# Kernel tuning notes

Hardware: AMD Instinct MI355X
Metric: run time of the kernel (lower is better)

Reference implementation:

```python
import jax, jax.numpy as jnp
import numpy as np

B, N, PS = 8, 2048, 32
P = N // PS          # 64 patches
D, MLP, DEPTH, H, DH = 1024, 2048, 6, 8, 64
INNER = H * DH       # 512
K = 20
EPS = 1e-5


def setup_inputs() -> dict:
    key = jax.random.key(0)
    ks = jax.random.split(key, 16)
    r = lambda i, shape: jax.random.normal(ks[i], shape, dtype=jnp.float32) * 0.02
    return {
        "x": jax.random.normal(ks[0], (B, N, 3), dtype=jnp.float32),
        "x_pos_embed": r(1, (B, P + 1, D)),
        "w1": r(2, (64, 6)),   "g1": jnp.ones(64),  "b1": jnp.zeros(64),
        "w2": r(3, (64, 128)), "g2": jnp.ones(64),  "b2": jnp.zeros(64),
        "w3": r(4, (128, 128)),"g3": jnp.ones(128), "b3": jnp.zeros(128),
        "w4": r(5, (256, 256)),"g4": jnp.ones(256), "b4": jnp.zeros(256),
        "w5": r(6, (D, 512)),  "g5": jnp.ones(D),   "b5": jnp.zeros(D),
        "cls_token": r(7, (1, 1, D)),
        "ln1_g": jnp.ones((DEPTH, D)), "ln1_b": jnp.zeros((DEPTH, D)),
        "wqkv": r(8, (DEPTH, D, 3 * INNER)),
        "wout": r(9, (DEPTH, INNER, D)), "bout": jnp.zeros((DEPTH, D)),
        "ln2_g": jnp.ones((DEPTH, D)), "ln2_b": jnp.zeros((DEPTH, D)),
        "wff1": r(10, (DEPTH, D, MLP)), "bff1": jnp.zeros((DEPTH, MLP)),
        "wff2": r(11, (DEPTH, MLP, D)), "bff2": jnp.zeros((DEPTH, D)),
    }


def _knn(x, k):  # x: [B, C, N] -> neighbor idx [B, N, k]
    xx = jnp.sum(x * x, axis=1)                        # [B, N]
    inner = jnp.einsum('bcn,bcm->bnm', x, x)           # [B, N, N]
    dist = 2.0 * inner - xx[:, :, None] - xx[:, None, :]  # = -||xi-xj||^2
    return jax.lax.top_k(dist, k)[1]


def _graph_feature(x, k):  # x: [B, C, N] -> [B, N, k, 2C]
    idx = _knn(x, k)
    xt = jnp.transpose(x, (0, 2, 1))                   # [B, N, C]
    nbr = jax.vmap(lambda f, i: f[i])(xt, idx)         # gather: [B, N, k, C]
    ctr = jnp.broadcast_to(xt[:, :, None, :], nbr.shape)
    return jnp.concatenate([nbr - ctr, ctr], axis=-1)


def _leaky(v):
    return jnp.where(v >= 0, v, 0.2 * v)


def _edge_conv(x, w, g, b, k):  # EdgeConv block: graph feat -> 1x1 conv -> BN(train) -> lrelu -> max over k
    f = _graph_feature(x, k)                           # [B, N, k, 2C]
    y = jnp.einsum('bnkc,oc->bonk', f, w)              # [B, O, N, k]
    mu = jnp.mean(y, axis=(0, 2, 3), keepdims=True)
    var = jnp.var(y, axis=(0, 2, 3), keepdims=True)
    y = (y - mu) * jax.lax.rsqrt(var + EPS) * g[None, :, None, None] + b[None, :, None, None]
    return jnp.max(_leaky(y), axis=-1)                 # [B, O, N]


def _ln(x, g, b):
    mu = jnp.mean(x, axis=-1, keepdims=True)
    var = jnp.var(x, axis=-1, keepdims=True)
    return (x - mu) * jax.lax.rsqrt(var + EPS) * g + b


def reference(x, x_pos_embed, w1, g1, b1, w2, g2, b2, w3, g3, b3, w4, g4, b4,
              w5, g5, b5, cls_token, ln1_g, ln1_b, wqkv, wout, bout,
              ln2_g, ln2_b, wff1, bff1, wff2, bff2):
    scale = DH ** -0.5
    pts = jnp.transpose(x, (0, 2, 1))                  # [B, 3, N]
    x1 = _edge_conv(pts, w1, g1, b1, K)                # [B, 64, N]
    x2 = _edge_conv(x1, w2, g2, b2, K)                 # [B, 64, N]
    x3 = _edge_conv(x2, w3, g3, b3, K)                 # [B, 128, N]
    x4 = _edge_conv(x3, w4, g4, b4, K)                 # [B, 256, N]
    h = jnp.concatenate([x1, x2, x3, x4], axis=1)      # [B, 512, N]
    y = jnp.einsum('bcn,oc->bon', h, w5)               # conv5 1x1 -> [B, D, N]
    mu = jnp.mean(y, axis=(0, 2), keepdims=True)
    var = jnp.var(y, axis=(0, 2), keepdims=True)
    y = _leaky((y - mu) * jax.lax.rsqrt(var + EPS) * g5[None, :, None] + b5[None, :, None])
    # patch max-pool: 'b (p n) c -> (b p) n c' then max over n
    t = jnp.transpose(y, (0, 2, 1)).reshape(B * P, PS, D)
    t = jnp.max(t, axis=1).reshape(B, P, D)
    t = jnp.concatenate([jnp.broadcast_to(cls_token, (B, 1, D)), t], axis=1)  # [B, P+1, D]
    for i in range(DEPTH):
        t = t + x_pos_embed
        hn = _ln(t, ln1_g[i], ln1_b[i])
        qkv = (hn @ wqkv[i]).reshape(B, P + 1, 3, H, DH)
        q, k_, v = [jnp.transpose(qkv[:, :, j], (0, 2, 1, 3)) for j in range(3)]
        attn = jax.nn.softmax(jnp.einsum('bhld,bhmd->bhlm', q, k_) * scale, axis=-1)
        z = jnp.einsum('bhlm,bhmd->bhld', attn, v)
        z = jnp.transpose(z, (0, 2, 1, 3)).reshape(B, P + 1, INNER)
        t = t + z @ wout[i] + bout[i]
        hn = _ln(t, ln2_g[i], ln2_b[i])
        t = t + jax.nn.gelu(hn @ wff1[i] + bff1[i], approximate=False) @ wff2[i] + bff2[i]
    return t[:, 1:]                                    # [B, P, D]
```

## Files before the change

kernel.cpp:

```cpp
#include <hip/hip_runtime.h>
#include <math.h>

#define BB 8
#define NN 2048
#define PSZ 32
#define PP 64
#define DD 1024
#define MLPD 2048
#define DEPTH_ 6
#define HH 8
#define DHH 64
#define INNER_ 512
#define KK 20
#define TOK 65
#define EPSF 1e-5f

#define GEMM_ACC 1
#define GEMM_GELU 2
#define GEMM_OUTBF16 4

typedef __bf16 bf16_t;
typedef __attribute__((ext_vector_type(8))) __bf16 bf16x8;
typedef __attribute__((ext_vector_type(4))) float f32x4;

__global__ void transpose_x_kernel(const float* __restrict__ x, float* __restrict__ pts) {
    int gid = blockIdx.x * blockDim.x + threadIdx.x;
    if (gid >= BB * NN * 3) return;
    int c = gid % 3; int n = (gid / 3) % NN; int b = gid / (3 * NN);
    pts[(b * 3 + c) * NN + n] = x[gid];
}

__global__ void sqnorm_kernel(const float* __restrict__ x, int bs, int C, float* __restrict__ xx) {
    int gid = blockIdx.x * blockDim.x + threadIdx.x;
    if (gid >= BB * NN) return;
    int n = gid % NN; int b = gid / NN;
    const float* xp = x + b * bs + n;
    float s = 0.f;
    for (int c = 0; c < C; ++c) { float v = xp[c * NN]; s += v * v; }
    xx[gid] = s;
}

__global__ __launch_bounds__(256) void dist_kernel(const float* __restrict__ x, int bs, int C,
                                                   const float* __restrict__ xx, int b0,
                                                   float* __restrict__ dist) {
    __shared__ float As[16][72];
    __shared__ float Bs[16][72];
    int b = b0 + blockIdx.z;
    int n0 = blockIdx.y * 64, m0 = blockIdx.x * 64;
    int tid = threadIdx.x;
    int ty = tid / 16, tx = tid % 16;
    float acc[4][4] = {};
    const float* xb = x + (long)b * bs;
    for (int k0 = 0; k0 < C; k0 += 16) {
        for (int ppp = 0; ppp < 4; ++ppp) {
            int li = tid + ppp * 256;
            int i = li % 64, kk = li / 64;
            int c = k0 + kk;
            As[kk][i] = (c < C) ? xb[c * NN + n0 + i] : 0.f;
            Bs[kk][i] = (c < C) ? xb[c * NN + m0 + i] : 0.f;
        }
        __syncthreads();
        for (int kk = 0; kk < 16; ++kk) {
            float a[4], bv[4];
            *(float4*)a = *(const float4*)&As[kk][ty * 4];
            *(float4*)bv = *(const float4*)&Bs[kk][tx * 4];
            for (int i2 = 0; i2 < 4; ++i2)
                for (int j = 0; j < 4; ++j)
                    acc[i2][j] += a[i2] * bv[j];
        }
        __syncthreads();
    }
    float* db = dist + (long)blockIdx.z * NN * NN;
    for (int i2 = 0; i2 < 4; ++i2) {
        int n = n0 + ty * 4 + i2;
        float xn = xx[b * NN + n];
        float4 st;
        int m = m0 + tx * 4;
        st.x = 2.f * acc[i2][0] - xn - xx[b * NN + m + 0];
        st.y = 2.f * acc[i2][1] - xn - xx[b * NN + m + 1];
        st.z = 2.f * acc[i2][2] - xn - xx[b * NN + m + 2];
        st.w = 2.f * acc[i2][3] - xn - xx[b * NN + m + 3];
        *(float4*)&db[(long)n * NN + m] = st;
    }
}

__global__ __launch_bounds__(256) void topk_kernel(const float* __restrict__ dist, int b0,
                                                   int* __restrict__ idx) {
    int b = b0 + blockIdx.y;
    int wid = threadIdx.x >> 6, lane = threadIdx.x & 63;
    int n = blockIdx.x * 4 + wid;
    const float* row = dist + ((long)blockIdx.y * NN + n) * NN;
    float vals[32];
    #pragma unroll
    for (int s = 0; s < 32; ++s) vals[s] = row[s * 64 + lane];
    int* op = idx + ((long)b * NN + n) * KK;
    for (int kk = 0; kk < KK; ++kk) {
        float bv = vals[0]; int bsl = 0;
        #pragma unroll
        for (int s = 1; s < 32; ++s) if (vals[s] > bv) { bv = vals[s]; bsl = s; }
        int bm = bsl * 64 + lane;
        for (int off = 32; off; off >>= 1) {
            float ov = __shfl_xor(bv, off);
            int om = __shfl_xor(bm, off);
            if (ov > bv || (ov == bv && om < bm)) { bv = ov; bm = om; }
        }
        int wslot = bm >> 6, wlane = bm & 63;
        #pragma unroll
        for (int s = 0; s < 32; ++s)
            if (s == wslot) vals[s] = (lane == wlane) ? -INFINITY : vals[s];
        if (lane == 0) op[kk] = bm;
    }
}

__global__ __launch_bounds__(256) void pq_kernel(const float* __restrict__ x, int bs, int C,
                                                 const float* __restrict__ w, int O,
                                                 float* __restrict__ p, float* __restrict__ q) {
    __shared__ float wT[256][33];
    __shared__ float xs[128][32];
    int b = blockIdx.z;
    int o0 = blockIdx.y * 32;
    int n0 = blockIdx.x * 32;
    int tid = threadIdx.x;
    for (int i = tid; i < 2 * C * 32; i += 256) {
        int c2 = i % (2 * C), o = i / (2 * C);
        wT[c2][o] = w[(o0 + o) * 2 * C + c2];
    }
    for (int i = tid; i < C * 32; i += 256) {
        int nl = i % 32, c = i / 32;
        xs[c][nl] = x[b * bs + c * NN + n0 + nl];
    }
    __syncthreads();
    int o_l = tid & 31;
    int n_base = (tid >> 5) * 4;
    float ps[4] = {0.f, 0.f, 0.f, 0.f};
    float qs[4] = {0.f, 0.f, 0.f, 0.f};
    for (int c = 0; c < C; ++c) {
        float4 xv = *(const float4*)&xs[c][n_base];
        float wa = wT[c][o_l];
        float wb = wT[C + c][o_l];
        float d = wb - wa;
        ps[0] += xv.x * wa; qs[0] += xv.x * d;
        ps[1] += xv.y * wa; qs[1] += xv.y * d;
        ps[2] += xv.z * wa; qs[2] += xv.z * d;
        ps[3] += xv.w * wa; qs[3] += xv.w * d;
    }
    for (int j = 0; j < 4; ++j) {
        long r = (long)(b * NN + n0 + n_base + j) * O + o0 + o_l;
        p[r] = ps[j];
        q[r] = qs[j];
    }
}

__global__ void zero_stats_kernel(double* __restrict__ s1, double* __restrict__ s2) {
    int t = blockIdx.x * blockDim.x + threadIdx.x;
    if (t < 1024) { s1[t] = 0.0; s2[t] = 0.0; }
}

__global__ __launch_bounds__(256) void edge_stats_kernel(const float* __restrict__ p, const float* __restrict__ q,
                                                         const int* __restrict__ idx, int O,
                                                         double* __restrict__ gsum, double* __restrict__ gsumsq) {
    int tid = threadIdx.x;
    int o = tid % O;
    int grp = tid / O;
    int ngrp = 256 / O;
    int rows_per_blk = (BB * NN) / gridDim.x;
    int r0 = blockIdx.x * rows_per_blk;
    double s = 0.0, ss = 0.0;
    for (int r = r0 + grp; r < r0 + rows_per_blk; r += ngrp) {
        int b = r / NN;
        float qv = q[r * O + o];
        for (int k = 0; k < KK; ++k) {
            int j = idx[r * KK + k];
            float v = p[(b * NN + j) * O + o] + qv;
            s += v; ss += (double)v * v;
        }
    }
    atomicAdd(&gsum[o], s);
    atomicAdd(&gsumsq[o], ss);
}

__global__ void bn_finalize_kernel(const double* __restrict__ gsum, const double* __restrict__ gsumsq,
                                   const float* __restrict__ g, const float* __restrict__ bb, int O, double cnt,
                                   float* __restrict__ scale, float* __restrict__ shift) {
    int o = blockIdx.x * blockDim.x + threadIdx.x;
    if (o >= O) return;
    double mean = gsum[o] / cnt;
    double var = gsumsq[o] / cnt - mean * mean;
    float inv = rsqrtf((float)var + EPSF);
    float sc = g[o] * inv;
    scale[o] = sc;
    shift[o] = bb[o] - (float)mean * sc;
}

__global__ void edge_out_kernel(const float* __restrict__ p, const float* __restrict__ q,
                                const int* __restrict__ idx, int O,
                                const float* __restrict__ scale, const float* __restrict__ shift,
                                float* __restrict__ out, int obs) {
    int gid = blockIdx.x * blockDim.x + threadIdx.x;
    if (gid >= BB * NN * O) return;
    int o = gid % O; int n = (gid / O) % NN; int b = gid / (O * NN);
    int r = b * NN + n;
    float qv = q[r * O + o];
    float sc = scale[o], sh = shift[o];
    float m = -INFINITY;
    for (int k = 0; k < KK; ++k) {
        int j = idx[r * KK + k];
        float v = (p[(b * NN + j) * O + o] + qv) * sc + sh;
        v = (v >= 0.f) ? v : 0.2f * v;
        m = fmaxf(m, v);
    }
    out[b * obs + o * NN + n] = m;
}

__global__ __launch_bounds__(256) void transpose_cvt_kernel(const float* __restrict__ in,
                                                            bf16_t* __restrict__ outp,
                                                            int R, int C, long s_in, long s_out) {
    __shared__ float tile[32][33];
    const float* ib = in + (long)blockIdx.z * s_in;
    bf16_t* ob = outp + (long)blockIdx.z * s_out;
    int r0 = blockIdx.y * 32, c0 = blockIdx.x * 32;
    int tx = threadIdx.x & 31, tg = threadIdx.x >> 5;
    for (int i = 0; i < 4; ++i) {
        int r = tg + i * 8;
        tile[r][tx] = ib[(long)(r0 + r) * C + c0 + tx];
    }
    __syncthreads();
    for (int i = 0; i < 4; ++i) {
        int c = tg + i * 8;
        ob[(long)(c0 + c) * R + r0 + tx] = (bf16_t)tile[tx][c];
    }
}

__global__ __launch_bounds__(256) void gemm_bf16_kernel(const float* __restrict__ A,
                                                        const bf16_t* __restrict__ Bt,
                                                        const float* __restrict__ bias,
                                                        float* __restrict__ out,
                                                        int M, int Kd, int Nd,
                                                        long sA, long sBt, long sO, int flags) {
    __shared__ __align__(16) bf16_t As[64 * 32];
    __shared__ __align__(16) bf16_t Bs[64 * 32];
    const float* Ab = A + (long)blockIdx.z * sA;
    const bf16_t* Bb = Bt + (long)blockIdx.z * sBt;
    int row0 = blockIdx.y * 64, col0 = blockIdx.x * 64;
    int tid = threadIdx.x;
    int lane = tid & 63, wv = tid >> 6;
    int wm = wv >> 1, wn = wv & 1;
    int srow = tid >> 2;
    int skp = (tid & 3) * 8;
    f32x4 acc[2][2] = {};
    for (int k0 = 0; k0 < Kd; k0 += 32) {
        {
            int r = row0 + srow;
            float av[8];
            if (r < M) {
                const float* ap = Ab + (long)r * Kd + k0 + skp;
                float4 a0 = *(const float4*)ap;
                float4 a1 = *(const float4*)(ap + 4);
                av[0] = a0.x; av[1] = a0.y; av[2] = a0.z; av[3] = a0.w;
                av[4] = a1.x; av[5] = a1.y; av[6] = a1.z; av[7] = a1.w;
            } else {
                #pragma unroll
                for (int j = 0; j < 8; ++j) av[j] = 0.f;
            }
            bf16x8 v;
            #pragma unroll
            for (int j = 0; j < 8; ++j) v[j] = (bf16_t)av[j];
            *(bf16x8*)&As[((skp >> 3) * 64 + srow) * 8] = v;
        }
        {
            const bf16_t* bp = Bb + (long)(col0 + srow) * Kd + k0 + skp;
            bf16x8 v = *(const bf16x8*)bp;
            *(bf16x8*)&Bs[((skp >> 3) * 64 + srow) * 8] = v;
        }
        __syncthreads();
        int q = lane >> 4, cl = lane & 15;
        bf16x8 a0v = *(const bf16x8*)&As[(q * 64 + wm * 32 + cl) * 8];
        bf16x8 a1v = *(const bf16x8*)&As[(q * 64 + wm * 32 + 16 + cl) * 8];
        bf16x8 b0v = *(const bf16x8*)&Bs[(q * 64 + wn * 32 + cl) * 8];
        bf16x8 b1v = *(const bf16x8*)&Bs[(q * 64 + wn * 32 + 16 + cl) * 8];
        acc[0][0] = __builtin_amdgcn_mfma_f32_16x16x32_bf16(a0v, b0v, acc[0][0], 0, 0, 0);
        acc[0][1] = __builtin_amdgcn_mfma_f32_16x16x32_bf16(a0v, b1v, acc[0][1], 0, 0, 0);
        acc[1][0] = __builtin_amdgcn_mfma_f32_16x16x32_bf16(a1v, b0v, acc[1][0], 0, 0, 0);
        acc[1][1] = __builtin_amdgcn_mfma_f32_16x16x32_bf16(a1v, b1v, acc[1][1], 0, 0, 0);
        __syncthreads();
    }
    int q = lane >> 4, cl = lane & 15;
    float* Obf = out + (long)blockIdx.z * sO;
    bf16_t* Obh = (bf16_t*)out + (long)blockIdx.z * sO;
    for (int mt = 0; mt < 2; ++mt)
        for (int nt = 0; nt < 2; ++nt)
            #pragma unroll
            for (int r = 0; r < 4; ++r) {
                int row = row0 + wm * 32 + mt * 16 + q * 4 + r;
                if (row >= M) continue;
                int col = col0 + wn * 32 + nt * 16 + cl;
                float v = acc[mt][nt][r];
                if (bias) v += bias[col];
                if (flags & GEMM_GELU) v = 0.5f * v * (1.f + erff(v * 0.70710678118654752f));
                long oidx = (long)row * Nd + col;
                if (flags & GEMM_OUTBF16) Obh[oidx] = (bf16_t)v;
                else if (flags & GEMM_ACC) Obf[oidx] += v;
                else Obf[oidx] = v;
            }
}

__global__ __launch_bounds__(256) void gemm_kernel(const float* __restrict__ A, const float* __restrict__ Bm,
                                                   const float* __restrict__ bias, float* __restrict__ out,
                                                   int M, int Kd, int Nd, long sA, long sB, long sO, int flags) {
    __shared__ float As[16][65];
    __shared__ float Bs[16][64];
    const float* Ab = A + (long)blockIdx.z * sA;
    const float* Bb = Bm + (long)blockIdx.z * sB;
    float* Ob = out + (long)blockIdx.z * sO;
    int row0 = blockIdx.y * 64, col0 = blockIdx.x * 64;
    int tid = threadIdx.x;
    int ty = tid / 16, tx = tid % 16;
    float acc[4][4] = {};
    for (int k0 = 0; k0 < Kd; k0 += 16) {
        for (int i = 0; i < 4; ++i) {
            int li = tid + i * 256;
            int m = li / 16, kk = li % 16;
            int r = row0 + m;
            As[kk][m] = (r < M) ? Ab[(long)r * Kd + k0 + kk] : 0.f;
        }
        for (int i = 0; i < 4; ++i) {
            int li = tid + i * 256;
            int kk = li / 64, n = li % 64;
            int c = col0 + n;
            Bs[kk][n] = (c < Nd) ? Bb[(long)(k0 + kk) * Nd + c] : 0.f;
        }
        __syncthreads();
        for (int kk = 0; kk < 16; ++kk) {
            float a[4], bv[4];
            for (int i = 0; i < 4; ++i) a[i] = As[kk][ty * 4 + i];
            for (int j = 0; j < 4; ++j) bv[j] = Bs[kk][tx * 4 + j];
            for (int i = 0; i < 4; ++i)
                for (int j = 0; j < 4; ++j)
                    acc[i][j] += a[i] * bv[j];
        }
        __syncthreads();
    }
    for (int i = 0; i < 4; ++i) {
        int r = row0 + ty * 4 + i;
        if (r >= M) continue;
        for (int j = 0; j < 4; ++j) {
            int c = col0 + tx * 4 + j;
            if (c >= Nd) continue;
            float v = acc[i][j];
            if (bias) v += bias[c];
            if (flags & GEMM_GELU) v = 0.5f * v * (1.f + erff(v * 0.70710678118654752f));
            long oidx = (long)r * Nd + c;
            if (flags & GEMM_ACC) Ob[oidx] += v; else Ob[oidx] = v;
        }
    }
}

__global__ __launch_bounds__(256) void bn5_stats_bf16_kernel(const bf16_t* __restrict__ y5,
                                                             const float* __restrict__ g,
                                                             const float* __restrict__ bb,
                                                             float* __restrict__ scale, float* __restrict__ shift) {
    __shared__ double ssum[256], ssq[256];
    int d = blockIdx.x;
    int tid = threadIdx.x;
    double s = 0.0, sq = 0.0;
    for (int b = 0; b < BB; ++b) {
        const bf16_t* row = y5 + ((long)b * DD + d) * NN;
        for (int n = tid; n < NN; n += 256) { float v = (float)row[n]; s += v; sq += (double)v * v; }
    }
    ssum[tid] = s; ssq[tid] = sq;
    __syncthreads();
    for (int st = 128; st > 0; st >>= 1) {
        if (tid < st) { ssum[tid] += ssum[tid + st]; ssq[tid] += ssq[tid + st]; }
        __syncthreads();
    }
    if (tid == 0) {
        double cnt = (double)BB * NN;
        double mean = ssum[0] / cnt;
        double var = ssq[0] / cnt - mean * mean;
        float inv = rsqrtf((float)var + EPSF);
        float sc = g[d] * inv;
        scale[d] = sc;
        shift[d] = bb[d] - (float)mean * sc;
    }
}

__global__ __launch_bounds__(256) void bn5_stats_kernel(const float* __restrict__ y5, const float* __restrict__ g,
                                                        const float* __restrict__ bb,
                                                        float* __restrict__ scale, float* __restrict__ shift) {
    __shared__ double ssum[256], ssq[256];
    int d = blockIdx.x;
    int tid = threadIdx.x;
    double s = 0.0, sq = 0.0;
    for (int b = 0; b < BB; ++b) {
        const float* row = y5 + ((long)b * DD + d) * NN;
        for (int n = tid; n < NN; n += 256) { float v = row[n]; s += v; sq += (double)v * v; }
    }
    ssum[tid] = s; ssq[tid] = sq;
    __syncthreads();
    for (int st = 128; st > 0; st >>= 1) {
        if (tid < st) { ssum[tid] += ssum[tid + st]; ssq[tid] += ssq[tid + st]; }
        __syncthreads();
    }
    if (tid == 0) {
        double cnt = (double)BB * NN;
        double mean = ssum[0] / cnt;
        double var = ssq[0] / cnt - mean * mean;
        float inv = rsqrtf((float)var + EPSF);
        float sc = g[d] * inv;
        scale[d] = sc;
        shift[d] = bb[d] - (float)mean * sc;
    }
}

__global__ void pool_bf16_kernel(const bf16_t* __restrict__ y5, const float* __restrict__ scale,
                                 const float* __restrict__ shift, const float* __restrict__ cls,
                                 float* __restrict__ t) {
    int gid = blockIdx.x * blockDim.x + threadIdx.x;
    if (gid >= BB * TOK * DD) return;
    int d = gid % DD; int l = (gid / DD) % TOK; int b = gid / (DD * TOK);
    float v;
    if (l == 0) {
        v = cls[d];
    } else {
        int pp = l - 1;
        const bf16_t* row = y5 + ((long)b * DD + d) * NN + pp * PSZ;
        float sc = scale[d], sh = shift[d];
        float m = -INFINITY;
        for (int i = 0; i < PSZ; ++i) {
            float u = (float)row[i] * sc + sh;
            u = (u >= 0.f) ? u : 0.2f * u;
            m = fmaxf(m, u);
        }
        v = m;
    }
    t[gid] = v;
}

__global__ void pool_kernel(const float* __restrict__ y5, const float* __restrict__ scale,
                            const float* __restrict__ shift, const float* __restrict__ cls,
                            float* __restrict__ t) {
    int gid = blockIdx.x * blockDim.x + threadIdx.x;
    if (gid >= BB * TOK * DD) return;
    int d = gid % DD; int l = (gid / DD) % TOK; int b = gid / (DD * TOK);
    float v;
    if (l == 0) {
        v = cls[d];
    } else {
        int pp = l - 1;
        const float* row = y5 + ((long)b * DD + d) * NN + pp * PSZ;
        float sc = scale[d], sh = shift[d];
        float m = -INFINITY;
        for (int i = 0; i < PSZ; ++i) {
            float u = row[i] * sc + sh;
            u = (u >= 0.f) ? u : 0.2f * u;
            m = fmaxf(m, u);
        }
        v = m;
    }
    t[gid] = v;
}

__global__ __launch_bounds__(256) void ln_kernel(float* __restrict__ t, const float* __restrict__ pos,
                                                 const float* __restrict__ g, const float* __restrict__ bb,
                                                 float* __restrict__ hn, int addpos) {
    __shared__ double s1[256], s2[256];
    long r = blockIdx.x;
    int tid = threadIdx.x;
    float vals[4];
    double s = 0.0, sq = 0.0;
    for (int i = 0; i < 4; ++i) {
        int d = tid + i * 256;
        float v = t[r * DD + d];
        if (addpos) { v += pos[r * DD + d]; t[r * DD + d] = v; }
        vals[i] = v; s += v; sq += (double)v * v;
    }
    s1[tid] = s; s2[tid] = sq;
    __syncthreads();
    for (int st = 128; st > 0; st >>= 1) {
        if (tid < st) { s1[tid] += s1[tid + st]; s2[tid] += s2[tid + st]; }
        __syncthreads();
    }
    double mean = s1[0] / DD;
    float var = (float)(s2[0] / DD - mean * mean);
    float fm = (float)mean;
    float inv = rsqrtf(var + EPSF);
    for (int i = 0; i < 4; ++i) {
        int d = tid + i * 256;
        hn[r * DD + d] = (vals[i] - fm) * inv * g[d] + bb[d];
    }
}

__global__ __launch_bounds__(256) void attn_kernel(const float* __restrict__ qkv, float* __restrict__ z) {
    __shared__ float ks[TOK][DHH + 1];
    __shared__ float vs[TOK][DHH + 1];
    __shared__ float ss[TOK][TOK];
    int bh = blockIdx.x;
    int b = bh / HH, h = bh % HH;
    int tid = threadIdx.x;
    for (int i = tid; i < TOK * DHH; i += 256) {
        int l = i / DHH, d = i % DHH;
        long base = (long)(b * TOK + l) * 1536;
        ks[l][d] = qkv[base + 512 + h * DHH + d];
        vs[l][d] = qkv[base + 1024 + h * DHH + d];
    }
    __syncthreads();
    for (int i = tid; i < TOK * TOK; i += 256) {
        int l = i / TOK, m = i % TOK;
        const float* qrow = qkv + (long)(b * TOK + l) * 1536 + h * DHH;
        float acc = 0.f;
        for (int d = 0; d < DHH; ++d) acc += qrow[d] * ks[m][d];
        ss[l][m] = acc * 0.125f;
    }
    __syncthreads();
    if (tid < TOK) {
        float mx = -INFINITY;
        for (int m = 0; m < TOK; ++m) mx = fmaxf(mx, ss[tid][m]);
        float sum = 0.f;
        for (int m = 0; m < TOK; ++m) { float e = expf(ss[tid][m] - mx); ss[tid][m] = e; sum += e; }
        float invs = 1.f / sum;
        for (int m = 0; m < TOK; ++m) ss[tid][m] *= invs;
    }
    __syncthreads();
    for (int i = tid; i < TOK * DHH; i += 256) {
        int l = i / DHH, d = i % DHH;
        float acc = 0.f;
        for (int m = 0; m < TOK; ++m) acc += ss[l][m] * vs[m][d];
        z[(long)(b * TOK + l) * INNER_ + h * DHH + d] = acc;
    }
}

__global__ void final_kernel(const float* __restrict__ t, float* __restrict__ out) {
    int gid = blockIdx.x * blockDim.x + threadIdx.x;
    if (gid >= BB * PP * DD) return;
    int d = gid % DD; int p = (gid / DD) % PP; int b = gid / (DD * PP);
    out[gid] = t[((long)b * TOK + 1 + p) * DD + d];
}

static inline int ceil_div(long a, long b) { return (int)((a + b - 1) / b); }

extern "C" void kernel_launch(void* const* d_in, const int* in_sizes, int n_in,
                              void* d_out, int out_size, void* d_ws, size_t ws_size,
                              hipStream_t stream) {
    const float* x    = (const float*)d_in[0];
    const float* pos  = (const float*)d_in[1];
    const float* w1   = (const float*)d_in[2];
    const float* g1   = (const float*)d_in[3];
    const float* b1   = (const float*)d_in[4];
    const float* w2   = (const float*)d_in[5];
    const float* g2   = (const float*)d_in[6];
    const float* b2   = (const float*)d_in[7];
    const float* w3   = (const float*)d_in[8];
    const float* g3   = (const float*)d_in[9];
    const float* b3   = (const float*)d_in[10];
    const float* w4   = (const float*)d_in[11];
    const float* g4   = (const float*)d_in[12];
    const float* b4   = (const float*)d_in[13];
    const float* w5   = (const float*)d_in[14];
    const float* g5   = (const float*)d_in[15];
    const float* b5   = (const float*)d_in[16];
    const float* cls  = (const float*)d_in[17];
    const float* ln1g = (const float*)d_in[18];
    const float* ln1b = (const float*)d_in[19];
    const float* wqkv = (const float*)d_in[20];
    const float* wout = (const float*)d_in[21];
    const float* bout = (const float*)d_in[22];
    const float* ln2g = (const float*)d_in[23];
    const float* ln2b = (const float*)d_in[24];
    const float* wff1 = (const float*)d_in[25];
    const float* bff1 = (const float*)d_in[26];
    const float* wff2 = (const float*)d_in[27];
    const float* bff2 = (const float*)d_in[28];
    float* out = (float*)d_out;

    char* ws = (char*)d_ws;
    size_t off = 0;
    auto alloc = [&](size_t bytes) -> char* {
        char* ptr = ws + off;
        off = (off + bytes + 255) & ~(size_t)255;
        return ptr;
    };
    float*  h      = (float*)alloc((size_t)BB * 512 * NN * 4);
    float*  t      = (float*)alloc((size_t)BB * TOK * DD * 4);
    float*  hn     = (float*)alloc((size_t)BB * TOK * DD * 4);
    float*  qkvb   = (float*)alloc((size_t)BB * TOK * 1536 * 4);
    float*  zb     = (float*)alloc((size_t)BB * TOK * INNER_ * 4);
    float*  ub     = (float*)alloc((size_t)BB * TOK * MLPD * 4);
    double* dsum   = (double*)alloc(1024 * 8);
    double* dsq    = (double*)alloc(1024 * 8);
    float*  scaleb = (float*)alloc(1024 * 4);
    float*  shiftb = (float*)alloc(1024 * 4);
    size_t ubase = off;

    size_t uoff = ubase;
    auto ualloc = [&](size_t bytes) -> char* {
        char* ptr = ws + uoff;
        uoff = (uoff + bytes + 255) & ~(size_t)255;
        return ptr;
    };
    float* pts  = (float*)ualloc((size_t)BB * 3 * NN * 4);
    float* xx   = (float*)ualloc((size_t)BB * NN * 4);
    int*   idxb = (int*)  ualloc((size_t)BB * NN * KK * 4);
    float* pbuf = (float*)ualloc((size_t)BB * NN * 256 * 4);
    float* qbuf = (float*)ualloc((size_t)BB * NN * 256 * 4);
    size_t dist_rel = uoff - ubase;
    float* distb = (float*)(ws + uoff);

    size_t voff = ubase;
    auto valloc = [&](size_t bytes) -> char* {
        char* ptr = ws + voff;
        voff = (voff + bytes + 255) & ~(size_t)255;
        return ptr;
    };
    bf16_t* hT     = (bf16_t*)valloc((size_t)BB * NN * 512 * 2);
    bf16_t* wTqkv  = (bf16_t*)valloc((size_t)DEPTH_ * 1536 * DD * 2);
    bf16_t* wTout  = (bf16_t*)valloc((size_t)DEPTH_ * DD * INNER_ * 2);
    bf16_t* wTff1  = (bf16_t*)valloc((size_t)DEPTH_ * MLPD * DD * 2);
    bf16_t* wTff2  = (bf16_t*)valloc((size_t)DEPTH_ * DD * MLPD * 2);
    size_t stage_bf16 = voff - ubase;

    size_t conv_full  = dist_rel + (size_t)BB * NN * NN * 4;
    size_t conv_batch = dist_rel + (size_t)NN * NN * 4;
    size_t stage_fp32 = (size_t)BB * DD * NN * 4;

    auto mx = [](size_t a, size_t b) { return a > b ? a : b; };
    bool use_bf16 = ws_size >= ubase + mx(conv_batch, stage_bf16);
    bool full     = ws_size >= ubase + mx(conv_full, use_bf16 ? stage_bf16 : stage_fp32);
    if (!use_bf16 && ws_size < ubase + mx(conv_batch, stage_fp32)) return;
    bf16_t* y5bf = (bf16_t*)h;
    float*  y5f  = (float*)(ws + ubase);

    transpose_x_kernel<<<ceil_div((long)BB * NN * 3, 256), 256, 0, stream>>>(x, pts);

    auto run_conv = [&](const float* xin, int xbs, int C, const float* w,
                        const float* g, const float* bb, float* hout, int O) {
        sqnorm_kernel<<<ceil_div((long)BB * NN, 256), 256, 0, stream>>>(xin, xbs, C, xx);
        if (full) {
            dist_kernel<<<dim3(NN / 64, NN / 64, BB), 256, 0, stream>>>(xin, xbs, C, xx, 0, distb);
            topk_kernel<<<dim3(NN / 4, BB), 256, 0, stream>>>(distb, 0, idxb);
        } else {
            for (int b = 0; b < BB; ++b) {
                dist_kernel<<<dim3(NN / 64, NN / 64, 1), 256, 0, stream>>>(xin, xbs, C, xx, b, distb);
                topk_kernel<<<dim3(NN / 4, 1), 256, 0, stream>>>(distb, b, idxb);
            }
        }
        {
            dim3 grid(NN / 32, O / 32, BB);
            pq_kernel<<<grid, 256, 0, stream>>>(xin, xbs, C, w, O, pbuf, qbuf);
        }
        zero_stats_kernel<<<4, 256, 0, stream>>>(dsum, dsq);
        edge_stats_kernel<<<256, 256, 0, stream>>>(pbuf, qbuf, idxb, O, dsum, dsq);
        bn_finalize_kernel<<<1, 256, 0, stream>>>(dsum, dsq, g, bb, O, (double)BB * NN * KK, scaleb, shiftb);
        edge_out_kernel<<<ceil_div((long)BB * NN * O, 256), 256, 0, stream>>>(
            pbuf, qbuf, idxb, O, scaleb, shiftb, hout, 512 * NN);
    };
    run_conv(pts, 3 * NN, 3, w1, g1, b1, h, 64);
    run_conv(h, 512 * NN, 64, w2, g2, b2, h + 64 * NN, 64);
    run_conv(h + 64 * NN, 512 * NN, 64, w3, g3, b3, h + 128 * NN, 128);
    run_conv(h + 128 * NN, 512 * NN, 128, w4, g4, b4, h + 256 * NN, 256);

    const int M = BB * TOK;
    if (use_bf16) {
        transpose_cvt_kernel<<<dim3(NN / 32, 512 / 32, BB), 256, 0, stream>>>(
            h, hT, 512, NN, (long)512 * NN, (long)NN * 512);
        transpose_cvt_kernel<<<dim3(1536 / 32, DD / 32, DEPTH_), 256, 0, stream>>>(
            wqkv, wTqkv, DD, 1536, (long)DD * 1536, (long)1536 * DD);
        transpose_cvt_kernel<<<dim3(DD / 32, INNER_ / 32, DEPTH_), 256, 0, stream>>>(
            wout, wTout, INNER_, DD, (long)INNER_ * DD, (long)DD * INNER_);
        transpose_cvt_kernel<<<dim3(MLPD / 32, DD / 32, DEPTH_), 256, 0, stream>>>(
            wff1, wTff1, DD, MLPD, (long)DD * MLPD, (long)MLPD * DD);
        transpose_cvt_kernel<<<dim3(DD / 32, MLPD / 32, DEPTH_), 256, 0, stream>>>(
            wff2, wTff2, MLPD, DD, (long)MLPD * DD, (long)DD * MLPD);

        gemm_bf16_kernel<<<dim3(NN / 64, DD / 64, BB), 256, 0, stream>>>(
            w5, hT, nullptr, (float*)y5bf, DD, 512, NN, 0L, (long)NN * 512, (long)DD * NN, GEMM_OUTBF16);
        bn5_stats_bf16_kernel<<<DD, 256, 0, stream>>>(y5bf, g5, b5, scaleb, shiftb);
        pool_bf16_kernel<<<ceil_div((long)BB * TOK * DD, 256), 256, 0, stream>>>(y5bf, scaleb, shiftb, cls, t);

        for (int i = 0; i < DEPTH_; ++i) {
            ln_kernel<<<M, 256, 0, stream>>>(t, pos, ln1g + i * DD, ln1b + i * DD, hn, 1);
            gemm_bf16_kernel<<<dim3(1536 / 64, ceil_div(M, 64), 1), 256, 0, stream>>>(
                hn, wTqkv + (size_t)i * 1536 * DD, nullptr, qkvb, M, DD, 1536, 0L, 0L, 0L, 0);
            attn_kernel<<<BB * HH, 256, 0, stream>>>(qkvb, zb);
            gemm_bf16_kernel<<<dim3(DD / 64, ceil_div(M, 64), 1), 256, 0, stream>>>(
                zb, wTout + (size_t)i * DD * INNER_, bout + i * DD, t, M, INNER_, DD, 0L, 0L, 0L, GEMM_ACC);
            ln_kernel<<<M, 256, 0, stream>>>(t, nullptr, ln2g + i * DD, ln2b + i * DD, hn, 0);
            gemm_bf16_kernel<<<dim3(MLPD / 64, ceil_div(M, 64), 1), 256, 0, stream>>>(
                hn, wTff1 + (size_t)i * MLPD * DD, bff1 + i * MLPD, ub, M, DD, MLPD, 0L, 0L, 0L, GEMM_GELU);
            gemm_bf16_kernel<<<dim3(DD / 64, ceil_div(M, 64), 1), 256, 0, stream>>>(
                ub, wTff2 + (size_t)i * DD * MLPD, bff2 + i * DD, t, M, MLPD, DD, 0L, 0L, 0L, GEMM_ACC);
        }
    } else {
        gemm_kernel<<<dim3(NN / 64, DD / 64, BB), 256, 0, stream>>>(
            w5, h, nullptr, y5f, DD, 512, NN, 0L, (long)512 * NN, (long)DD * NN, 0);
        bn5_stats_kernel<<<DD, 256, 0, stream>>>(y5f, g5, b5, scaleb, shiftb);
        pool_kernel<<<ceil_div((long)BB * TOK * DD, 256), 256, 0, stream>>>(y5f, scaleb, shiftb, cls, t);
        for (int i = 0; i < DEPTH_; ++i) {
            ln_kernel<<<M, 256, 0, stream>>>(t, pos, ln1g + i * DD, ln1b + i * DD, hn, 1);
            gemm_kernel<<<dim3(1536 / 64, ceil_div(M, 64), 1), 256, 0, stream>>>(
                hn, wqkv + (size_t)i * DD * 1536, nullptr, qkvb, M, DD, 1536, 0L, 0L, 0L, 0);
            attn_kernel<<<BB * HH, 256, 0, stream>>>(qkvb, zb);
            gemm_kernel<<<dim3(DD / 64, ceil_div(M, 64), 1), 256, 0, stream>>>(
                zb, wout + (size_t)i * INNER_ * DD, bout + i * DD, t, M, INNER_, DD, 0L, 0L, 0L, GEMM_ACC);
            ln_kernel<<<M, 256, 0, stream>>>(t, nullptr, ln2g + i * DD, ln2b + i * DD, hn, 0);
            gemm_kernel<<<dim3(MLPD / 64, ceil_div(M, 64), 1), 256, 0, stream>>>(
                hn, wff1 + (size_t)i * DD * MLPD, bff1 + i * MLPD, ub, M, DD, MLPD, 0L, 0L, 0L, GEMM_GELU);
            gemm_kernel<<<dim3(DD / 64, ceil_div(M, 64), 1), 256, 0, stream>>>(
                ub, wff2 + (size_t)i * MLPD * DD, bff2 + i * DD, t, M, MLPD, DD, 0L, 0L, 0L, GEMM_ACC);
        }
    }

    final_kernel<<<ceil_div((long)BB * PP * DD, 256), 256, 0, stream>>>(t, out);
}
```

Before: 2.441 ms.

## Fuse kNN distance computation with streaming top-k selection

Replaces the separate distance GEMM (which wrote an N×N fp32 matrix per batch) and the 20-pass top-k kernel with one kernel. It computes distance tiles in shared memory and keeps a running sorted top-20 list per row in wave lanes, inserting candidates only when they beat the current 20th-best threshold. This removes the large dist buffer traffic and its workspace requirement. The cost is serialized ballot-and-shuffle insertion work and a grid of only 256 blocks per layer, which may limit parallelism early on when the thresholds are still loose.

```diff
diff --git a/kernel.cpp b/kernel.cpp
--- a/kernel.cpp
+++ b/kernel.cpp
@@ -40,75 +40,104 @@
     xx[gid] = s;
 }
 
-__global__ __launch_bounds__(256) void dist_kernel(const float* __restrict__ x, int bs, int C,
-                                                   const float* __restrict__ xx, int b0,
-                                                   float* __restrict__ dist) {
-    __shared__ float As[16][72];
-    __shared__ float Bs[16][72];
-    int b = b0 + blockIdx.z;
-    int n0 = blockIdx.y * 64, m0 = blockIdx.x * 64;
-    int tid = threadIdx.x;
-    int ty = tid / 16, tx = tid % 16;
-    float acc[4][4] = {};
+__device__ __forceinline__ float knn_insert(float& lv, int& li, float cv, int cm, int lane) {
+    unsigned long long geq = __ballot(lane < 20 && (lv > cv || (lv == cv && li < cm)));
+    int r = __popcll(geq);
+    float pv = __shfl_up(lv, 1);
+    int   pi = __shfl_up(li, 1);
+    if (lane >= r && lane < 20) {
+        lv = (lane == r) ? cv : pv;
+        li = (lane == r) ? cm : pi;
+    }
+    return __shfl(lv, 19);
+}
+
+__global__ __launch_bounds__(512) void knn_fused_kernel(const float* __restrict__ x, int bs, int C,
+                                                        const float* __restrict__ xx,
+                                                        int* __restrict__ idx) {
+    __shared__ float As[128][64];
+    __shared__ float Bs[128][64];
+    int b = blockIdx.y;
+    int n0 = blockIdx.x * 64;
+    int tid = threadIdx.x;
+    int lane = tid & 63;
+    int w = tid >> 6;
+    int ty = tid >> 4;
+    int tx = tid & 15;
     const float* xb = x + (long)b * bs;
-    for (int k0 = 0; k0 < C; k0 += 16) {
-        for (int ppp = 0; ppp < 4; ++ppp) {
-            int li = tid + ppp * 256;
-            int i = li % 64, kk = li / 64;
-            int c = k0 + kk;
-            As[kk][i] = (c < C) ? xb[c * NN + n0 + i] : 0.f;
-            Bs[kk][i] = (c < C) ? xb[c * NN + m0 + i] : 0.f;
-        }
-        __syncthreads();
-        for (int kk = 0; kk < 16; ++kk) {
-            float a[4], bv[4];
-            *(float4*)a = *(const float4*)&As[kk][ty * 4];
-            *(float4*)bv = *(const float4*)&Bs[kk][tx * 4];
-            for (int i2 = 0; i2 < 4; ++i2)
-                for (int j = 0; j < 4; ++j)
-                    acc[i2][j] += a[i2] * bv[j];
-        }
-        __syncthreads();
-    }
-    float* db = dist + (long)blockIdx.z * NN * NN;
-    for (int i2 = 0; i2 < 4; ++i2) {
-        int n = n0 + ty * 4 + i2;
-        float xn = xx[b * NN + n];
-        float4 st;
-        int m = m0 + tx * 4;
-        st.x = 2.f * acc[i2][0] - xn - xx[b * NN + m + 0];
-        st.y = 2.f * acc[i2][1] - xn - xx[b * NN + m + 1];
-        st.z = 2.f * acc[i2][2] - xn - xx[b * NN + m + 2];
-        st.w = 2.f * acc[i2][3] - xn - xx[b * NN + m + 3];
-        *(float4*)&db[(long)n * NN + m] = st;
-    }
-}
-
-__global__ __launch_bounds__(256) void topk_kernel(const float* __restrict__ dist, int b0,
-                                                   int* __restrict__ idx) {
-    int b = b0 + blockIdx.y;
-    int wid = threadIdx.x >> 6, lane = threadIdx.x & 63;
-    int n = blockIdx.x * 4 + wid;
-    const float* row = dist + ((long)blockIdx.y * NN + n) * NN;
-    float vals[32];
+    for (int e = tid; e < C * 64; e += 512) {
+        int c = e >> 6, n = e & 63;
+        As[c][n] = xb[c * NN + n0 + n];
+    }
+    float xn0 = xx[b * NN + n0 + ty * 2];
+    float xn1 = xx[b * NN + n0 + ty * 2 + 1];
+    float lval[8]; int lidx[8];
     #pragma unroll
-    for (int s = 0; s < 32; ++s) vals[s] = row[s * 64 + lane];
-    int* op = idx + ((long)b * NN + n) * KK;
-    for (int kk = 0; kk < KK; ++kk) {
-        float bv = vals[0]; int bsl = 0;
+    for (int r = 0; r < 8; ++r) { lval[r] = -INFINITY; lidx[r] = 1 << 30; }
+    float thr0 = -INFINITY, thr1 = -INFINITY;
+    for (int m0 = 0; m0 < NN; m0 += 64) {
+        __syncthreads();
+        for (int e = tid; e < C * 64; e += 512) {
+            int c = e >> 6, n = e & 63;
+            Bs[c][n] = xb[c * NN + m0 + n];
+        }
+        __syncthreads();
+        float acc[2][4] = {};
+        for (int c = 0; c < C; ++c) {
+            float2 a = *(const float2*)&As[c][ty * 2];
+            float4 bv = *(const float4*)&Bs[c][tx * 4];
+            acc[0][0] += a.x * bv.x; acc[0][1] += a.x * bv.y; acc[0][2] += a.x * bv.z; acc[0][3] += a.x * bv.w;
+            acc[1][0] += a.y * bv.x; acc[1][1] += a.y * bv.y; acc[1][2] += a.y * bv.z; acc[1][3] += a.y * bv.w;
+        }
+        float4 xm4 = *(const float4*)&xx[b * NN + m0 + tx * 4];
+        float xmv[4] = {xm4.x, xm4.y, xm4.z, xm4.w};
         #pragma unroll
-        for (int s = 1; s < 32; ++s) if (vals[s] > bv) { bv = vals[s]; bsl = s; }
-        int bm = bsl * 64 + lane;
-        for (int off = 32; off; off >>= 1) {
-            float ov = __shfl_xor(bv, off);
-            int om = __shfl_xor(bm, off);
-            if (ov > bv || (ov == bv && om < bm)) { bv = ov; bm = om; }
-        }
-        int wslot = bm >> 6, wlane = bm & 63;
+        for (int i = 0; i < 2; ++i) {
+            float thr = i ? thr1 : thr0;
+            float xni = i ? xn1 : xn0;
+            float dv[4];
+            #pragma unroll
+            for (int j = 0; j < 4; ++j) dv[j] = 2.f * acc[i][j] - xni - xmv[j];
+            unsigned long long mj0 = __ballot(dv[0] > thr);
+            unsigned long long mj1 = __ballot(dv[1] > thr);
+            unsigned long long mj2 = __ballot(dv[2] > thr);
+            unsigned long long mj3 = __ballot(dv[3] > thr);
+            unsigned long long any = mj0 | mj1 | mj2 | mj3;
+            while (any) {
+                int l = __ffsll((long long)any) - 1;
+                any &= any - 1;
+                int g_c = l >> 4;
+                int rc = (g_c << 1) + i;
+                #pragma unroll
+                for (int j = 0; j < 4; ++j) {
+                    unsigned long long mj = (j == 0) ? mj0 : (j == 1) ? mj1 : (j == 2) ? mj2 : mj3;
+                    if (!((mj >> l) & 1)) continue;
+                    float cv = __shfl(dv[j], l);
+                    int cm = m0 + ((l & 15) << 2) + j;
+                    float cur = __shfl(i ? thr1 : thr0, g_c << 4);
+                    if (!(cv > cur)) continue;
+                    float thrnew;
+                    switch (rc) {
+                        case 0: thrnew = knn_insert(lval[0], lidx[0], cv, cm, lane); break;
+                        case 1: thrnew = knn_insert(lval[1], lidx[1], cv, cm, lane); break;
+                        case 2: thrnew = knn_insert(lval[2], lidx[2], cv, cm, lane); break;
+                        case 3: thrnew = knn_insert(lval[3], lidx[3], cv, cm, lane); break;
+                        case 4: thrnew = knn_insert(lval[4], lidx[4], cv, cm, lane); break;
+                        case 5: thrnew = knn_insert(lval[5], lidx[5], cv, cm, lane); break;
+                        case 6: thrnew = knn_insert(lval[6], lidx[6], cv, cm, lane); break;
+                        default: thrnew = knn_insert(lval[7], lidx[7], cv, cm, lane); break;
+                    }
+                    if ((lane >> 4) == g_c) { if (i) thr1 = thrnew; else thr0 = thrnew; }
+                }
+            }
+        }
+    }
+    if (lane < 20) {
         #pragma unroll
-        for (int s = 0; s < 32; ++s)
-            if (s == wslot) vals[s] = (lane == wlane) ? -INFINITY : vals[s];
-        if (lane == 0) op[kk] = bm;
+        for (int rc = 0; rc < 8; ++rc) {
+            int n = n0 + w * 8 + rc;
+            idx[((long)b * NN + n) * KK + lane] = lidx[rc];
+        }
     }
 }
 
@@ -602,8 +631,7 @@
     int*   idxb = (int*)  ualloc((size_t)BB * NN * KK * 4);
     float* pbuf = (float*)ualloc((size_t)BB * NN * 256 * 4);
     float* qbuf = (float*)ualloc((size_t)BB * NN * 256 * 4);
-    size_t dist_rel = uoff - ubase;
-    float* distb = (float*)(ws + uoff);
+    size_t conv_sz = uoff - ubase;
 
     size_t voff = ubase;
     auto valloc = [&](size_t bytes) -> char* {
@@ -618,14 +646,11 @@
     bf16_t* wTff2  = (bf16_t*)valloc((size_t)DEPTH_ * DD * MLPD * 2);
     size_t stage_bf16 = voff - ubase;
 
-    size_t conv_full  = dist_rel + (size_t)BB * NN * NN * 4;
-    size_t conv_batch = dist_rel + (size_t)NN * NN * 4;
     size_t stage_fp32 = (size_t)BB * DD * NN * 4;
 
     auto mx = [](size_t a, size_t b) { return a > b ? a : b; };
-    bool use_bf16 = ws_size >= ubase + mx(conv_batch, stage_bf16);
-    bool full     = ws_size >= ubase + mx(conv_full, use_bf16 ? stage_bf16 : stage_fp32);
-    if (!use_bf16 && ws_size < ubase + mx(conv_batch, stage_fp32)) return;
+    bool use_bf16 = ws_size >= ubase + mx(conv_sz, stage_bf16);
+    if (!use_bf16 && ws_size < ubase + mx(conv_sz, stage_fp32)) return;
     bf16_t* y5bf = (bf16_t*)h;
     float*  y5f  = (float*)(ws + ubase);
 
@@ -634,15 +659,7 @@
     auto run_conv = [&](const float* xin, int xbs, int C, const float* w,
                         const float* g, const float* bb, float* hout, int O) {
         sqnorm_kernel<<<ceil_div((long)BB * NN, 256), 256, 0, stream>>>(xin, xbs, C, xx);
-        if (full) {
-            dist_kernel<<<dim3(NN / 64, NN / 64, BB), 256, 0, stream>>>(xin, xbs, C, xx, 0, distb);
-            topk_kernel<<<dim3(NN / 4, BB), 256, 0, stream>>>(distb, 0, idxb);
-        } else {
-            for (int b = 0; b < BB; ++b) {
-                dist_kernel<<<dim3(NN / 64, NN / 64, 1), 256, 0, stream>>>(xin, xbs, C, xx, b, distb);
-                topk_kernel<<<dim3(NN / 4, 1), 256, 0, stream>>>(distb, b, idxb);
-            }
-        }
+        knn_fused_kernel<<<dim3(NN / 64, BB), 512, 0, stream>>>(xin, xbs, C, xx, idxb);
         {
             dim3 grid(NN / 32, O / 32, BB);
             pq_kernel<<<grid, 256, 0, stream>>>(xin, xbs, C, w, O, pbuf, qbuf);
```

Result: slower. 3.828 ms (+56.8%).
